# Performance work log

Measured on AMD Instinct MI355X. Metric: run time of the kernel, lower is better.

## Reference

```python
import jax, jax.numpy as jnp
import numpy as np

D_MODEL = 1024
NUM_HEADS = 16
D_IN = 1024

def setup_inputs() -> dict:
    key = jax.random.key(0)
    ks = jax.random.split(key, 5)
    scale = 1.0 / np.sqrt(D_IN)
    return {
        "in_features": jax.random.normal(ks[0], (4, 2048, D_IN), dtype=jnp.float32),
        "q_weight": jax.random.normal(ks[1], (D_MODEL, D_IN), dtype=jnp.float32) * scale,
        "k_weight": jax.random.normal(ks[2], (D_MODEL, D_IN), dtype=jnp.float32) * scale,
        "v_weight": jax.random.normal(ks[3], (D_MODEL, D_IN), dtype=jnp.float32) * scale,
        "o_weight": jax.random.normal(ks[4], (D_MODEL, D_MODEL), dtype=jnp.float32) * scale,
    }

def reference(in_features, q_weight, k_weight, v_weight, o_weight):
    batch, seq_len, _ = in_features.shape
    d_head = D_MODEL // NUM_HEADS
    # QKV projections (Linear with no bias: x @ W^T)
    q = jnp.einsum('bsi,di->bsd', in_features, q_weight)
    k = jnp.einsum('bsi,di->bsd', in_features, k_weight)
    v = jnp.einsum('bsi,di->bsd', in_features, v_weight)
    # split heads -> [b, h, s, d_head]
    q = q.reshape(batch, seq_len, NUM_HEADS, d_head).transpose(0, 2, 1, 3)
    k = k.reshape(batch, seq_len, NUM_HEADS, d_head).transpose(0, 2, 1, 3)
    v = v.reshape(batch, seq_len, NUM_HEADS, d_head).transpose(0, 2, 1, 3)
    # scaled dot-product attention (scale by per-head dim, as in SelfAttention)
    scores = jnp.einsum('bhqd,bhkd->bhqk', q, k) / jnp.sqrt(jnp.float32(d_head))
    probs = jax.nn.softmax(scores, axis=-1)
    ctx = jnp.einsum('bhqk,bhkd->bhqd', probs, v)
    # merge heads -> [b, s, d_model]
    ctx = ctx.transpose(0, 2, 1, 3).reshape(batch, seq_len, D_MODEL)
    # output projection
    return jnp.einsum('bsd,md->bsm', ctx, o_weight)
```

## Files before the change

kernel.cpp:

```cpp
#include <hip/hip_runtime.h>

typedef _Float16 half8 __attribute__((ext_vector_type(8)));
typedef _Float16 half4v __attribute__((ext_vector_type(4)));
typedef __fp16 fp16x2 __attribute__((ext_vector_type(2)));
typedef float f32x4 __attribute__((ext_vector_type(4)));
typedef float f32x16 __attribute__((ext_vector_type(16)));

__device__ __forceinline__ void gload_lds16(const _Float16* g, _Float16* l) {
    __builtin_amdgcn_global_load_lds(
        (const __attribute__((address_space(1))) void*)g,
        (__attribute__((address_space(3))) void*)l,
        16, 0, 0);
}

__global__ void cvt_f32_f16(const float* __restrict__ src, _Float16* __restrict__ dst, int n4) {
    int i = blockIdx.x * blockDim.x + threadIdx.x;
    if (i >= n4) return;
    f32x4 v = ((const f32x4*)src)[i];
    half4v h;
    h[0] = (_Float16)v[0]; h[1] = (_Float16)v[1];
    h[2] = (_Float16)v[2]; h[3] = (_Float16)v[3];
    ((half4v*)dst)[i] = h;
}

__global__ void cvt4_f32_f16(const float* __restrict__ s0, const float* __restrict__ s1,
                             const float* __restrict__ s2, const float* __restrict__ s3,
                             _Float16* __restrict__ dst) {
    int i = blockIdx.x * blockDim.x + threadIdx.x;
    int wsel = blockIdx.y;
    const float* src = (wsel == 0) ? s0 : (wsel == 1) ? s1 : (wsel == 2) ? s2 : s3;
    f32x4 v = ((const f32x4*)src)[i];
    half4v h;
    h[0] = (_Float16)v[0]; h[1] = (_Float16)v[1];
    h[2] = (_Float16)v[2]; h[3] = (_Float16)v[3];
    ((half4v*)(dst + (size_t)wsel * 1048576))[i] = h;
}

template<int MODE>
__global__ void gemm_nt(const _Float16* __restrict__ A,
                        const _Float16* __restrict__ Wbase,
                        void* __restrict__ outbase)
{
    constexpr int K = 1024;
    __shared__ _Float16 As[2][128 * 32];
    __shared__ _Float16 Bs[2][128 * 32];

    const int tid  = threadIdx.x;
    const int lane = tid & 63;
    const int w    = tid >> 6;
    const int wr   = w >> 1, wc = w & 1;
    const int lr   = lane & 15, lg = lane >> 4;

    int brow, bcol, mat;
    {
        const int wg = blockIdx.x;
        const int k = wg & 7, i = wg >> 3;
        if (MODE == 0) {
            const int x = i / 3;
            const int ypanel = 3 * k + (i - 3 * x);
            brow = x * 128;
            mat  = ypanel >> 3;
            bcol = (ypanel & 7) * 128;
        } else {
            brow = i * 128;
            bcol = k * 128;
            mat  = 0;
        }
    }

    const _Float16* Bw = Wbase + (MODE == 0 ? (size_t)mat * (1024u * 1024u) : 0);

    const int srow = w * 16 + (lane >> 2);
    const int scol = (lane & 3) * 8;
    const _Float16* Ag = A  + (size_t)(brow + srow) * K + scol;
    const _Float16* Bg = Bw + (size_t)(bcol + srow) * K + scol;

    auto stage = [&](int buf, int kt) {
        const _Float16* a0 = Ag + kt * 32;
        const _Float16* b0 = Bg + kt * 32;
        gload_lds16(a0,           &As[buf][w * 512]);
        gload_lds16(a0 + 64 * K,  &As[buf][w * 512 + 2048]);
        gload_lds16(b0,           &Bs[buf][w * 512]);
        gload_lds16(b0 + 64 * K,  &Bs[buf][w * 512 + 2048]);
    };

    f32x4 acc[4][4] = {};
    stage(0, 0);
    __syncthreads();

    for (int kt = 0; kt < K / 32; ++kt) {
        const int cur = kt & 1;
        if (kt + 1 < K / 32) stage(cur ^ 1, kt + 1);
        half8 af[4], bf[4];
#pragma unroll
        for (int mi = 0; mi < 4; ++mi)
            af[mi] = *(const half8*)&As[cur][(wr * 64 + mi * 16 + lr) * 32 + lg * 8];
#pragma unroll
        for (int ni = 0; ni < 4; ++ni)
            bf[ni] = *(const half8*)&Bs[cur][(wc * 64 + ni * 16 + lr) * 32 + lg * 8];
#pragma unroll
        for (int mi = 0; mi < 4; ++mi)
#pragma unroll
            for (int ni = 0; ni < 4; ++ni)
                acc[mi][ni] = __builtin_amdgcn_mfma_f32_16x16x32_f16(af[mi], bf[ni], acc[mi][ni], 0, 0, 0);
        __syncthreads();
    }

    if (MODE == 0) {
        _Float16* outp = (_Float16*)outbase + (size_t)mat * (8192u * 1024u);
        if (mat == 2) {
            _Float16* Ts = &As[0][0];
#pragma unroll
            for (int p = 0; p < 2; ++p) {
                if (wc == p) {
#pragma unroll
                    for (int mi = 0; mi < 4; ++mi)
#pragma unroll
                        for (int ni = 0; ni < 4; ++ni) {
                            int drow = ni * 16 + lr;
                            int s0   = wr * 64 + mi * 16 + lg * 4;
                            half4v o;
#pragma unroll
                            for (int r = 0; r < 4; ++r) o[r] = (_Float16)acc[mi][ni][r];
                            int byteoff = drow * 256 + s0 * 2;
                            byteoff ^= (drow & 7) << 4;
                            *(half4v*)((char*)Ts + byteoff) = o;
                        }
                }
                __syncthreads();
                {
                    int row   = tid >> 2;
                    int cbase = (tid & 3) * 4;
                    int gd = bcol + p * 64 + row;
                    int h = gd >> 6, dd = gd & 63;
                    int b = brow >> 11, sseq = brow & 2047;
                    _Float16* gout = outp + (((size_t)b * 16 + h) * 64 + dd) * 2048 + sseq;
#pragma unroll
                    for (int j = 0; j < 4; ++j) {
                        int c  = cbase + j;
                        int lc = c ^ (row & 7);
                        half8 v = *(const half8*)&Ts[row * 128 + lc * 8];
                        *(half8*)&gout[c * 8] = v;
                    }
                }
                __syncthreads();
            }
        } else {
            const float scale = (mat == 0) ? 0.18033688f : 1.0f;
#pragma unroll
            for (int mi = 0; mi < 4; ++mi)
#pragma unroll
                for (int ni = 0; ni < 4; ++ni)
#pragma unroll
                    for (int r = 0; r < 4; ++r) {
                        int row = brow + wr * 64 + mi * 16 + lg * 4 + r;
                        int col = bcol + wc * 64 + ni * 16 + lr;
                        int b = row >> 11, s = row & 2047;
                        int h = col >> 6,  d = col & 63;
                        outp[(((size_t)b * 16 + h) * 2048 + s) * 64 + d] =
                            (_Float16)(acc[mi][ni][r] * scale);
                    }
        }
    } else {
        float* outp = (float*)outbase;
#pragma unroll
        for (int mi = 0; mi < 4; ++mi)
#pragma unroll
            for (int ni = 0; ni < 4; ++ni)
#pragma unroll
                for (int r = 0; r < 4; ++r) {
                    int row = brow + wr * 64 + mi * 16 + lg * 4 + r;
                    int col = bcol + wc * 64 + ni * 16 + lr;
                    outp[(size_t)row * 1024 + col] = acc[mi][ni][r];
                }
    }
}

#define M_FIX 10.0f
__global__ __launch_bounds__(256, 4)
void attn_kernel(const _Float16* __restrict__ Q,
                 const _Float16* __restrict__ Kx,
                 const _Float16* __restrict__ Vt,
                 _Float16* __restrict__ Ctx)
{
    __shared__ _Float16 Ks[2][64 * 72];
    __shared__ _Float16 Vs[2][64 * 72];

    const int tid = threadIdx.x, lane = tid & 63, w = tid >> 6;
    const int l31 = lane & 31, hi = lane >> 5;

    const int wg = blockIdx.x;
    const int j = ((wg & 7) << 7) + (wg >> 3);
    const int bh = j >> 4, qblk = j & 15;

    const _Float16* Qp  = Q  + ((size_t)bh * 2048 + qblk * 128) * 64;
    const _Float16* Kp  = Kx + (size_t)bh * 2048 * 64;
    const _Float16* Vtp = Vt + (size_t)bh * 64 * 2048;

    half8 qf[4];
#pragma unroll
    for (int ks = 0; ks < 4; ++ks)
        qf[ks] = *(const half8*)(Qp + (size_t)(w * 32 + l31) * 64 + ks * 16 + hi * 8);

    const int srow = tid >> 3;
    const int scol = (tid & 7) * 8;
    const _Float16* Kg0 = Kp  + (size_t)srow * 64   + scol;
    const _Float16* Vg0 = Vtp + (size_t)srow * 2048 + scol;
    const int ldso = srow * 72 + scol;

    const fp16x2 ones2 = {(__fp16)1.0f, (__fp16)1.0f};

    f32x16 cacc[2] = {};
    float l0 = 0.f, l1 = 0.f;

    half8 kr0, kr1, vr0, vr1;
    kr0 = *(const half8*)(Kg0);
    kr1 = *(const half8*)(Kg0 + 2048);
    vr0 = *(const half8*)(Vg0);
    vr1 = *(const half8*)(Vg0 + 32 * 2048);
    *(half8*)&Ks[0][ldso]           = kr0;
    *(half8*)&Ks[0][ldso + 32 * 72] = kr1;
    *(half8*)&Vs[0][ldso]           = vr0;
    *(half8*)&Vs[0][ldso + 32 * 72] = vr1;
    __syncthreads();

    for (int t = 0; t < 32; ++t) {
        const int cur = t & 1;
        if (t < 31) {
            kr0 = *(const half8*)(Kg0 + (size_t)(t + 1) * 4096);
            kr1 = *(const half8*)(Kg0 + (size_t)(t + 1) * 4096 + 2048);
        }

        f32x16 sf[2];
        __builtin_amdgcn_s_setprio(1);
#pragma unroll
        for (int kt = 0; kt < 2; ++kt) {
            f32x16 z;
#pragma unroll
            for (int r = 0; r < 16; ++r) z[r] = -M_FIX;
#pragma unroll
            for (int ks = 0; ks < 4; ++ks) {
                half8 kf = *(const half8*)&Ks[cur][(kt * 32 + l31) * 72 + ks * 16 + hi * 8];
                z = __builtin_amdgcn_mfma_f32_32x32x16_f16(kf, qf[ks], z, 0, 0, 0);
            }
            sf[kt] = z;
        }
        __builtin_amdgcn_s_setprio(0);

        if (t < 31) {
            *(half8*)&Ks[cur ^ 1][ldso]           = kr0;
            *(half8*)&Ks[cur ^ 1][ldso + 32 * 72] = kr1;
            vr0 = *(const half8*)(Vg0 + (t + 1) * 64);
            vr1 = *(const half8*)(Vg0 + (t + 1) * 64 + 32 * 2048);
        }

        half8 bf[4];
#pragma unroll
        for (int kt = 0; kt < 2; ++kt) {
#pragma unroll
            for (int r = 0; r < 16; ++r)
                sf[kt][r] = __builtin_amdgcn_exp2f(sf[kt][r]);

            unsigned uq[4][2];
#pragma unroll
            for (int qd = 0; qd < 4; ++qd)
#pragma unroll
                for (int w2 = 0; w2 < 2; ++w2)
                    uq[qd][w2] = __builtin_bit_cast(unsigned,
                        __builtin_amdgcn_cvt_pkrtz(sf[kt][4 * qd + 2 * w2],
                                                   sf[kt][4 * qd + 2 * w2 + 1]));

#pragma unroll
            for (int k1 = 0; k1 < 2; ++k1) {
                union { half8 h; unsigned u[4]; } bu;
#pragma unroll
                for (int w2 = 0; w2 < 2; ++w2) {
                    unsigned a = uq[2 * k1][w2];
                    unsigned b = uq[2 * k1 + 1][w2];
                    asm("v_permlane32_swap_b32 %0, %1" : "+v"(a), "+v"(b));
                    bu.u[w2]     = a;
                    bu.u[2 + w2] = b;
                }
                l0 = __builtin_amdgcn_fdot2(__builtin_bit_cast(fp16x2, bu.u[0]), ones2, l0, false);
                l1 = __builtin_amdgcn_fdot2(__builtin_bit_cast(fp16x2, bu.u[1]), ones2, l1, false);
                l0 = __builtin_amdgcn_fdot2(__builtin_bit_cast(fp16x2, bu.u[2]), ones2, l0, false);
                l1 = __builtin_amdgcn_fdot2(__builtin_bit_cast(fp16x2, bu.u[3]), ones2, l1, false);
                bf[kt * 2 + k1] = bu.h;
            }
        }

        __builtin_amdgcn_s_setprio(1);
#pragma unroll
        for (int dt = 0; dt < 2; ++dt)
#pragma unroll
            for (int ks = 0; ks < 4; ++ks) {
                half8 vf = *(const half8*)&Vs[cur][(dt * 32 + l31) * 72 + ks * 16 + hi * 8];
                cacc[dt] = __builtin_amdgcn_mfma_f32_32x32x16_f16(vf, bf[ks], cacc[dt], 0, 0, 0);
            }
        __builtin_amdgcn_s_setprio(0);

        if (t < 31) {
            *(half8*)&Vs[cur ^ 1][ldso]           = vr0;
            *(half8*)&Vs[cur ^ 1][ldso + 32 * 72] = vr1;
        }
        __syncthreads();
    }

    float l = l0 + l1;
    const float inv = 1.0f / (l + __shfl_xor(l, 32, 64));
    const int s = qblk * 128 + w * 32 + l31;
    _Float16* Cp = Ctx + ((size_t)(bh >> 4) * 2048 + s) * 1024 + (bh & 15) * 64;
#pragma unroll
    for (int dt = 0; dt < 2; ++dt)
#pragma unroll
        for (int qd = 0; qd < 4; ++qd) {
            half4v o;
#pragma unroll
            for (int j2 = 0; j2 < 4; ++j2) o[j2] = (_Float16)(cacc[dt][4 * qd + j2] * inv);
            *(half4v*)&Cp[dt * 32 + qd * 8 + hi * 4] = o;
        }
}

extern "C" void kernel_launch(void* const* d_in, const int* in_sizes, int n_in,
                              void* d_out, int out_size, void* d_ws, size_t ws_size,
                              hipStream_t stream)
{
    const float* X  = (const float*)d_in[0];
    const float* Wq = (const float*)d_in[1];
    const float* Wk = (const float*)d_in[2];
    const float* Wv = (const float*)d_in[3];
    const float* Wo = (const float*)d_in[4];

    if (ws_size < (size_t)(8 + 4 + 24) * 1024 * 1024 * 2) return;
    _Float16* Xh  = (_Float16*)d_ws;
    _Float16* Wh  = Xh + (size_t)8 * 1024 * 1024;
    _Float16* QKV = Wh + (size_t)4 * 1024 * 1024;
    _Float16* Ctx = Xh;

    cvt_f32_f16<<<8192, 256, 0, stream>>>(X, Xh, 2097152);
    cvt4_f32_f16<<<dim3(1024, 4), 256, 0, stream>>>(Wq, Wk, Wv, Wo, Wh);

    gemm_nt<0><<<1536, 256, 0, stream>>>(Xh, Wh, QKV);

    attn_kernel<<<1024, 256, 0, stream>>>(QKV, QKV + 8388608, QKV + 16777216, Ctx);

    gemm_nt<1><<<512, 256, 0, stream>>>(Ctx, Wh + 3145728, d_out);
}
```

Measured before the change: 205.7 us.

## Fuse conversion kernels, simplify GEMM grid mapping, stage Q/K epilogue via LDS

The two fp32-to-fp16 conversion kernels are merged into one launch covering the input and all four weights, which saves a kernel launch. The GEMMs drop the swizzled workgroup-to-tile mapping in favour of a plain 3D grid. That may cost L2 locality, since the old scheme grouped tiles that share weight panels. The Q/K epilogue now writes through a swizzled LDS tile so the global stores become 16-byte coalesced vectors instead of scattered 2-byte writes, at the price of extra barriers.

```diff
diff --git a/kernel.cpp b/kernel.cpp
--- a/kernel.cpp
+++ b/kernel.cpp
@@ -13,27 +13,28 @@
         16, 0, 0);
 }
 
-__global__ void cvt_f32_f16(const float* __restrict__ src, _Float16* __restrict__ dst, int n4) {
+__global__ void cvt_all(const float* __restrict__ X,
+                        const float* __restrict__ W0, const float* __restrict__ W1,
+                        const float* __restrict__ W2, const float* __restrict__ W3,
+                        _Float16* __restrict__ Xh, _Float16* __restrict__ Wh) {
     int i = blockIdx.x * blockDim.x + threadIdx.x;
-    if (i >= n4) return;
-    f32x4 v = ((const f32x4*)src)[i];
+    const float* src;
+    _Float16* dst;
+    int idx;
+    if (i < 2097152) {
+        src = X; dst = Xh; idx = i;
+    } else {
+        int j = i - 2097152;
+        int wsel = j >> 18;
+        idx = j & 262143;
+        src = (wsel == 0) ? W0 : (wsel == 1) ? W1 : (wsel == 2) ? W2 : W3;
+        dst = Wh + (size_t)wsel * 1048576;
+    }
+    f32x4 v = ((const f32x4*)src)[idx];
     half4v h;
     h[0] = (_Float16)v[0]; h[1] = (_Float16)v[1];
     h[2] = (_Float16)v[2]; h[3] = (_Float16)v[3];
-    ((half4v*)dst)[i] = h;
-}
-
-__global__ void cvt4_f32_f16(const float* __restrict__ s0, const float* __restrict__ s1,
-                             const float* __restrict__ s2, const float* __restrict__ s3,
-                             _Float16* __restrict__ dst) {
-    int i = blockIdx.x * blockDim.x + threadIdx.x;
-    int wsel = blockIdx.y;
-    const float* src = (wsel == 0) ? s0 : (wsel == 1) ? s1 : (wsel == 2) ? s2 : s3;
-    f32x4 v = ((const f32x4*)src)[i];
-    half4v h;
-    h[0] = (_Float16)v[0]; h[1] = (_Float16)v[1];
-    h[2] = (_Float16)v[2]; h[3] = (_Float16)v[3];
-    ((half4v*)(dst + (size_t)wsel * 1048576))[i] = h;
+    ((half4v*)dst)[idx] = h;
 }
 
 template<int MODE>
@@ -50,25 +51,11 @@
     const int w    = tid >> 6;
     const int wr   = w >> 1, wc = w & 1;
     const int lr   = lane & 15, lg = lane >> 4;
-
-    int brow, bcol, mat;
-    {
-        const int wg = blockIdx.x;
-        const int k = wg & 7, i = wg >> 3;
-        if (MODE == 0) {
-            const int x = i / 3;
-            const int ypanel = 3 * k + (i - 3 * x);
-            brow = x * 128;
-            mat  = ypanel >> 3;
-            bcol = (ypanel & 7) * 128;
-        } else {
-            brow = i * 128;
-            bcol = k * 128;
-            mat  = 0;
-        }
-    }
-
-    const _Float16* Bw = Wbase + (MODE == 0 ? (size_t)mat * (1024u * 1024u) : 0);
+    const int brow = blockIdx.x * 128;
+    const int bcol = blockIdx.y * 128;
+    const int mat  = (MODE == 0) ? blockIdx.z : 0;
+
+    const _Float16* Bw = Wbase + (size_t)mat * (1024u * 1024u);
 
     const int srow = w * 16 + (lane >> 2);
     const int scol = (lane & 3) * 8;
@@ -108,8 +95,8 @@
 
     if (MODE == 0) {
         _Float16* outp = (_Float16*)outbase + (size_t)mat * (8192u * 1024u);
+        _Float16* Ts = &As[0][0];
         if (mat == 2) {
-            _Float16* Ts = &As[0][0];
 #pragma unroll
             for (int p = 0; p < 2; ++p) {
                 if (wc == p) {
@@ -148,18 +135,37 @@
         } else {
             const float scale = (mat == 0) ? 0.18033688f : 1.0f;
 #pragma unroll
-            for (int mi = 0; mi < 4; ++mi)
-#pragma unroll
-                for (int ni = 0; ni < 4; ++ni)
-#pragma unroll
-                    for (int r = 0; r < 4; ++r) {
-                        int row = brow + wr * 64 + mi * 16 + lg * 4 + r;
-                        int col = bcol + wc * 64 + ni * 16 + lr;
-                        int b = row >> 11, s = row & 2047;
-                        int h = col >> 6,  d = col & 63;
-                        outp[(((size_t)b * 16 + h) * 2048 + s) * 64 + d] =
-                            (_Float16)(acc[mi][ni][r] * scale);
+            for (int p = 0; p < 2; ++p) {
+                if (wr == p) {
+#pragma unroll
+                    for (int mi = 0; mi < 4; ++mi)
+#pragma unroll
+                        for (int ni = 0; ni < 4; ++ni)
+#pragma unroll
+                            for (int r = 0; r < 4; ++r) {
+                                int rloc = mi * 16 + lg * 4 + r;
+                                int cloc = wc * 64 + ni * 16 + lr;
+                                Ts[rloc * 128 + (cloc ^ ((rloc & 15) << 3))] =
+                                    (_Float16)(acc[mi][ni][r] * scale);
+                            }
+                }
+                __syncthreads();
+                {
+                    int rloc = tid >> 2;
+                    int cb   = (tid & 3) * 32;
+                    int row  = brow + p * 64 + rloc;
+                    int b = row >> 11, s = row & 2047;
+#pragma unroll
+                    for (int j = 0; j < 4; ++j) {
+                        int c0  = cb + j * 8;
+                        int col = bcol + c0;
+                        int h = col >> 6, d = col & 63;
+                        half8 v = *(const half8*)&Ts[rloc * 128 + (c0 ^ ((rloc & 15) << 3))];
+                        *(half8*)&outp[(((size_t)b * 16 + h) * 2048 + s) * 64 + d] = v;
                     }
+                }
+                __syncthreads();
+            }
         }
     } else {
         float* outp = (float*)outbase;
@@ -337,12 +343,11 @@
     _Float16* QKV = Wh + (size_t)4 * 1024 * 1024;
     _Float16* Ctx = Xh;
 
-    cvt_f32_f16<<<8192, 256, 0, stream>>>(X, Xh, 2097152);
-    cvt4_f32_f16<<<dim3(1024, 4), 256, 0, stream>>>(Wq, Wk, Wv, Wo, Wh);
-
-    gemm_nt<0><<<1536, 256, 0, stream>>>(Xh, Wh, QKV);
+    cvt_all<<<12288, 256, 0, stream>>>(X, Wq, Wk, Wv, Wo, Xh, Wh);
+
+    gemm_nt<0><<<dim3(64, 8, 3), 256, 0, stream>>>(Xh, Wh, QKV);
 
     attn_kernel<<<1024, 256, 0, stream>>>(QKV, QKV + 8388608, QKV + 16777216, Ctx);
 
-    gemm_nt<1><<<512, 256, 0, stream>>>(Ctx, Wh + 3145728, d_out);
-}
+    gemm_nt<1><<<dim3(64, 8), 256, 0, stream>>>(Ctx, Wh + 3145728, d_out);
+}
```

Measured after the change: 200.7 us. 2.4% less time.
